# Kernel optimization log

Measured on AMD Instinct MI355X. Metric: run time of the kernel, lower is better.

## Reference

```python
import jax, jax.numpy as jnp
import numpy as np

B, C, H, W = 32, 256, 56, 56
O, K = 512, 3


def setup_inputs() -> dict:
    key = jax.random.key(0)
    kx, kw = jax.random.split(key)
    x = jax.random.normal(kx, (B, C, H, W), dtype=jnp.float32)
    # Ternary weight stored as two disjoint boolean masks of shape (C*K*K, O),
    # matching the torch buffer layout: weight.view(O, C*K*K).t().
    u = jax.random.uniform(kw, (C * K * K, O))
    pos_weight = u < 0.45
    neg_weight = u > 0.55
    return {"x": x, "pos_weight": pos_weight, "neg_weight": neg_weight}


def reference(x, pos_weight, neg_weight):
    # pos/neg masks: (C*K*K, O) bool, disjoint. The torch module computes
    # sum(unfold(x) where pos) - sum(unfold(x) where neg) over the C*K*K axis
    # per output channel, i.e. a conv with ternary weight in {-1, 0, +1}.
    b, c, h, w = x.shape
    ckk, o = pos_weight.shape
    k = int(round((ckk // c) ** 0.5))  # kernel size (square)
    wt = pos_weight.astype(x.dtype) - neg_weight.astype(x.dtype)  # (C*K*K, O)
    # torch unfold orders the patch axis as (C, kh, kw); weight came from
    # view(O, C*K*K).t(), so transposing back gives OIHW layout directly.
    wt = wt.T.reshape(o, c, k, k)
    pad = (k - 1) // 2  # 'same' padding (output reshaped to (b, O, h, w))
    out = jax.lax.conv_general_dilated(
        x, wt,
        window_strides=(1, 1),
        padding=[(pad, pad), (pad, pad)],
        dimension_numbers=("NCHW", "OIHW", "NCHW"),
    )
    return out  # (b, O, h, w)
```

## Files before the change

kernel.cpp:

```cpp
#include <hip/hip_runtime.h>
#include <hip/hip_bf16.h>

#define BB 32
#define CC 256
#define HH 56
#define WW 56
#define OO 512
#define CKK 2304

#define XR 58
#define XC 58
#define XPIX (XR * XC)

#define NY 4
#define NX 28
#define NTILE 112
#define TPC 30
#define TPIX 180
#define BUFB 16384

typedef __bf16 bf16x8 __attribute__((ext_vector_type(8)));
typedef float  f32x4  __attribute__((ext_vector_type(4)));

#define WT_OFF 4096
#define XP_OFF (WT_OFF + (size_t)OO * CKK * 2)

__global__ void detect_bool_width(const unsigned int* __restrict__ pos,
                                  unsigned int* __restrict__ flag) {
    unsigned int v = 0;
    for (int i = threadIdx.x; i < 16384; i += 256) v |= pos[i];
    __shared__ unsigned int red;
    if (threadIdx.x == 0) red = 0u;
    __syncthreads();
    if (v > 1u) atomicOr(&red, 1u);
    __syncthreads();
    if (threadIdx.x == 0) *flag = red;
}

__global__ __launch_bounds__(256) void decode_w(
    const void* __restrict__ posv, const void* __restrict__ negv,
    const unsigned int* __restrict__ flag,
    unsigned short* __restrict__ wt) {
    __shared__ unsigned short lds[64][65];
    int blk = blockIdx.x;
    int ot  = blk & 7;
    int khw = (blk >> 3) % 9;
    int ct  = blk / 72;
    int o0 = ot * 64, c0 = ct * 64;
    int t = threadIdx.x;
    int o_l = t & 63, row4 = t >> 6;
    bool bytes = (*flag != 0u);
#pragma unroll
    for (int r = 0; r < 16; ++r) {
        int c_l = row4 + r * 4;
        long k = (long)(c0 + c_l) * 9 + khw;
        long idx = k * OO + o0 + o_l;
        int p, q;
        if (bytes) { p = ((const unsigned char*)posv)[idx];
                     q = ((const unsigned char*)negv)[idx]; }
        else       { p = ((const int*)posv)[idx];
                     q = ((const int*)negv)[idx]; }
        lds[c_l][o_l] = p ? 0x3F80u : (q ? 0xBF80u : 0u);
    }
    __syncthreads();
#pragma unroll
    for (int r = 0; r < 16; ++r) {
        int o_r = row4 + r * 4;
        int c = c0 + (t & 63);
        wt[(size_t)(o0 + o_r) * CKK + (c >> 5) * 288 + khw * 32 + (c & 31)] =
            lds[t & 63][o_r];
    }
}

__global__ __launch_bounds__(256) void pad_x(const float* __restrict__ x,
                                             unsigned short* __restrict__ xp) {
    int blk = blockIdx.x;
    int b = blk / XR, y = blk - b * XR;
    int t = threadIdx.x;
    unsigned short* rowp = xp + ((size_t)b * XPIX + (size_t)y * XC) * CC;
    if (y == 0 || y == XR - 1) {
        uint4 z = {0, 0, 0, 0};
        for (int i = t; i < XC * CC / 8; i += 256) ((uint4*)rowp)[i] = z;
        return;
    }
    __shared__ float lds[WW][65];
    for (int cb = 0; cb < 4; ++cb) {
        if (cb) __syncthreads();
#pragma unroll
        for (int i = 0; i < 14; ++i) {
            int idx = i * 256 + t;
            int cl = idx / WW, xx = idx - cl * WW;
            lds[xx][cl] =
                x[(((size_t)b * CC + cb * 64 + cl) * HH + (y - 1)) * WW + xx];
        }
        __syncthreads();
#pragma unroll
        for (int i = 0; i < 15; ++i) {
            int idx = i * 256 + t;
            if (idx < XC * 64) {
                int xx = idx >> 6, cl = idx & 63;
                float v = (xx == 0 || xx == XC - 1) ? 0.f : lds[xx - 1][cl];
                __hip_bfloat16 h = __float2bfloat16(v);
                rowp[(size_t)xx * CC + cb * 64 + cl] = *(unsigned short*)&h;
            }
        }
    }
}

__global__ __launch_bounds__(256, 2) void conv_mfma(
    const unsigned short* __restrict__ xp,
    const unsigned short* __restrict__ wt,
    float* __restrict__ out) {
    __shared__ __align__(1024) unsigned short Bs[2 * BUFB / 2];

    int t = threadIdx.x;
    int w = t >> 6, lane = t & 63, lm = lane & 15, lq = lane >> 4;

    int bx = blockIdx.x;
    int mb = (bx >> 3) & 1;
    int gn = ((bx >> 4) << 3) | (bx & 7);
    int b = gn / 28;
    int rem = gn - b * 28;
    int y0 = (rem >> 1) << 2;
    int x0 = (rem & 1) * NX;

    int bofs[7];
#pragma unroll
    for (int nt = 0; nt < 7; ++nt) {
        int n = nt * 16 + lm;
        int ny = n / NX, nx = n - (n / NX) * NX;
        bofs[nt] = (ny * TPC + nx) * 64 + lq * 16;
    }

    const unsigned short* gsrc[3];
    int useg[3];
#pragma unroll
    for (int i = 0; i < 3; ++i) {
        int u = (w * 3 + i) * 64 + lane;
        useg[i] = u;
        int pix = u >> 2, quad = u & 3;
        int py = pix / TPC, px = pix - py * TPC;
        gsrc[i] = xp + ((size_t)b * XPIX + (y0 + py) * XC + (x0 + px)) * CC +
                  quad * 8;
    }
    int ldsseg = (w * 3) * 1024;

    const unsigned short* aptr[4];
#pragma unroll
    for (int mt = 0; mt < 4; ++mt)
        aptr[mt] = wt + (size_t)(mb * 256 + w * 64 + mt * 16 + lm) * CKK + lq * 8;

    f32x4 acc[4][7];
#pragma unroll
    for (int i = 0; i < 4; ++i)
#pragma unroll
        for (int j = 0; j < 7; ++j) acc[i][j] = (f32x4){0.f, 0.f, 0.f, 0.f};

    bf16x8 af[12];

#define STAGE(CHOFF, POFS)                                                     \
    {                                                                          \
        _Pragma("unroll") for (int i = 0; i < 3; ++i) {                        \
            if (useg[i] < TPIX * 4)                                            \
                __builtin_amdgcn_global_load_lds(                              \
                    (const __attribute__((address_space(1))) void*)(gsrc[i] +  \
                                                                    (CHOFF)),  \
                    (__attribute__((address_space(3))) void*)((char*)Bs +      \
                                                              (POFS) + ldsseg +\
                                                              i * 1024),       \
                    16, 0, 0);                                                 \
        }                                                                      \
    }

#define LOADA(CHEL, G)                                                         \
    {                                                                          \
        _Pragma("unroll") for (int j = 0; j < 3; ++j)                          \
            _Pragma("unroll") for (int mt = 0; mt < 4; ++mt)                   \
                af[j * 4 + mt] = *(const bf16x8*)(aptr[mt] + (CHEL) +          \
                                                  ((G) * 3 + j) * 32);         \
    }

#define GRP(G, POFS)                                                           \
    {                                                                          \
        _Pragma("unroll") for (int j = 0; j < 3; ++j) {                        \
            const int khw = (G) * 3 + j;                                       \
            const int kh = khw / 3, kw = khw - kh * 3;                         \
            _Pragma("unroll") for (int nt = 0; nt < 7; ++nt) {                 \
                bf16x8 bfr = *(const bf16x8*)((char*)Bs + (POFS) +             \
                                              (kh * TPC + kw) * 64 + bofs[nt]);\
                _Pragma("unroll") for (int mt = 0; mt < 4; ++mt)               \
                    acc[mt][nt] = __builtin_amdgcn_mfma_f32_16x16x32_bf16(     \
                        af[j * 4 + mt], bfr, acc[mt][nt], 0, 0, 0);            \
            }                                                                  \
        }                                                                      \
    }

    STAGE(0, 0);
    LOADA(0, 0);
    for (int it = 0; it < 4; ++it) {
        __syncthreads();
        STAGE(32, BUFB);
        GRP(0, 0);
        LOADA(0, 1);  GRP(1, 0);
        LOADA(0, 2);  GRP(2, 0);
        LOADA(288, 0);
        __syncthreads();
        if (it < 3) STAGE(64, 0);
        GRP(0, BUFB);
        LOADA(288, 1); GRP(1, BUFB);
        LOADA(288, 2); GRP(2, BUFB);
        if (it < 3) {
#pragma unroll
            for (int mt = 0; mt < 4; ++mt) aptr[mt] += 576;
#pragma unroll
            for (int i = 0; i < 3; ++i) gsrc[i] += 64;
            LOADA(0, 0);
        }
    }
#undef STAGE
#undef LOADA
#undef GRP

#pragma unroll
    for (int mt = 0; mt < 4; ++mt) {
        int o = mb * 256 + w * 64 + mt * 16 + lq * 4;
#pragma unroll
        for (int nt = 0; nt < 7; ++nt) {
            int n = nt * 16 + lm;
            int ny = n / NX, nx = n - (n / NX) * NX;
            size_t base =
                (((size_t)b * OO + o) * HH + (y0 + ny)) * WW + (x0 + nx);
#pragma unroll
            for (int r = 0; r < 4; ++r)
                out[base + (size_t)r * HH * WW] = acc[mt][nt][r];
        }
    }
}

extern "C" void kernel_launch(void* const* d_in, const int* in_sizes, int n_in,
                              void* d_out, int out_size, void* d_ws, size_t ws_size,
                              hipStream_t stream) {
    const float* x   = (const float*)d_in[0];
    const void*  pos = d_in[1];
    const void*  neg = d_in[2];
    float* out = (float*)d_out;

    unsigned int* flag = (unsigned int*)d_ws;
    unsigned short* wt = (unsigned short*)((char*)d_ws + WT_OFF);
    unsigned short* xpad = (unsigned short*)((char*)d_ws + XP_OFF);

    detect_bool_width<<<1, 256, 0, stream>>>((const unsigned int*)pos, flag);
    decode_w<<<288, 256, 0, stream>>>(pos, neg, flag, wt);
    pad_x<<<BB * XR, 256, 0, stream>>>(x, xpad);
    conv_mfma<<<dim3(1792), 256, 0, stream>>>(xpad, wt, out);
}
```

Before: 616.5 us.

## Pad LDS pixel stride and stage input via registers instead of direct LDS loads

Moves staging of the input tile from global_load_lds direct-to-LDS copies to ordinary global loads into registers, followed by explicit ds_write stores spread across the MFMA groups. The LDS pixel stride is padded from 64 to 80 bytes so that B-fragment reads from LDS hit fewer bank conflicts, which the fixed-layout direct loads could not provide. The cost is extra VGPRs to hold the staged data and extra LDS write instructions, which may hurt occupancy or scheduling.

Result: slower. 716.8 us (+16.3%).

```diff
diff --git a/kernel.cpp b/kernel.cpp
--- a/kernel.cpp
+++ b/kernel.cpp
@@ -17,6 +17,7 @@
 #define NTILE 112
 #define TPC 30
 #define TPIX 180
+#define PSTR 80
 #define BUFB 16384
 
 typedef __bf16 bf16x8 __attribute__((ext_vector_type(8)));
@@ -129,21 +130,20 @@
     for (int nt = 0; nt < 7; ++nt) {
         int n = nt * 16 + lm;
         int ny = n / NX, nx = n - (n / NX) * NX;
-        bofs[nt] = (ny * TPC + nx) * 64 + lq * 16;
-    }
-
+        bofs[nt] = (ny * TPC + nx) * PSTR + lq * 16;
+    }
+
+    int u0 = w * 192 + lane;
     const unsigned short* gsrc[3];
-    int useg[3];
 #pragma unroll
     for (int i = 0; i < 3; ++i) {
-        int u = (w * 3 + i) * 64 + lane;
-        useg[i] = u;
-        int pix = u >> 2, quad = u & 3;
+        int u = u0 + 64 * i;
+        int pix = u >> 2, q = u & 3;
         int py = pix / TPC, px = pix - py * TPC;
         gsrc[i] = xp + ((size_t)b * XPIX + (y0 + py) * XC + (x0 + px)) * CC +
-                  quad * 8;
-    }
-    int ldsseg = (w * 3) * 1024;
+                  q * 8;
+    }
+    int wadr0 = (u0 >> 2) * PSTR + (u0 & 3) * 16;
 
     const unsigned short* aptr[4];
 #pragma unroll
@@ -157,19 +157,25 @@
         for (int j = 0; j < 7; ++j) acc[i][j] = (f32x4){0.f, 0.f, 0.f, 0.f};
 
     bf16x8 af[12];
-
-#define STAGE(CHOFF, POFS)                                                     \
-    {                                                                          \
-        _Pragma("unroll") for (int i = 0; i < 3; ++i) {                        \
-            if (useg[i] < TPIX * 4)                                            \
-                __builtin_amdgcn_global_load_lds(                              \
-                    (const __attribute__((address_space(1))) void*)(gsrc[i] +  \
-                                                                    (CHOFF)),  \
-                    (__attribute__((address_space(3))) void*)((char*)Bs +      \
-                                                              (POFS) + ldsseg +\
-                                                              i * 1024),       \
-                    16, 0, 0);                                                 \
-        }                                                                      \
+    bf16x8 s0, s1, s2;
+
+#define GLOAD01(CHOFF)                                                         \
+    {                                                                          \
+        s0 = *(const bf16x8*)(gsrc[0] + (CHOFF));                              \
+        if (u0 < 656) s1 = *(const bf16x8*)(gsrc[1] + (CHOFF));                \
+    }
+#define GLOAD2(CHOFF)                                                          \
+    {                                                                          \
+        if (u0 < 592) s2 = *(const bf16x8*)(gsrc[2] + (CHOFF));                \
+    }
+#define DSW01(POFS)                                                            \
+    {                                                                          \
+        *(bf16x8*)((char*)Bs + (POFS) + wadr0) = s0;                           \
+        if (u0 < 656) *(bf16x8*)((char*)Bs + (POFS) + wadr0 + 1280) = s1;      \
+    }
+#define DSW2(POFS)                                                             \
+    {                                                                          \
+        if (u0 < 592) *(bf16x8*)((char*)Bs + (POFS) + wadr0 + 2560) = s2;      \
     }
 
 #define LOADA(CHEL, G)                                                         \
@@ -187,7 +193,8 @@
             const int kh = khw / 3, kw = khw - kh * 3;                         \
             _Pragma("unroll") for (int nt = 0; nt < 7; ++nt) {                 \
                 bf16x8 bfr = *(const bf16x8*)((char*)Bs + (POFS) +             \
-                                              (kh * TPC + kw) * 64 + bofs[nt]);\
+                                              (kh * TPC + kw) * PSTR +         \
+                                              bofs[nt]);                       \
                 _Pragma("unroll") for (int mt = 0; mt < 4; ++mt)               \
                     acc[mt][nt] = __builtin_amdgcn_mfma_f32_16x16x32_bf16(     \
                         af[j * 4 + mt], bfr, acc[mt][nt], 0, 0, 0);            \
@@ -195,21 +202,29 @@
         }                                                                      \
     }
 
-    STAGE(0, 0);
+    GLOAD01(0); GLOAD2(0);
+    DSW01(0);   DSW2(0);
     LOADA(0, 0);
     for (int it = 0; it < 4; ++it) {
         __syncthreads();
-        STAGE(32, BUFB);
+        GLOAD01(32);
         GRP(0, 0);
-        LOADA(0, 1);  GRP(1, 0);
-        LOADA(0, 2);  GRP(2, 0);
+        LOADA(0, 1); GLOAD2(32);
+        GRP(1, 0);
+        DSW01(BUFB);
+        LOADA(0, 2); GRP(2, 0);
+        DSW2(BUFB);
         LOADA(288, 0);
         __syncthreads();
-        if (it < 3) STAGE(64, 0);
+        if (it < 3) GLOAD01(64);
         GRP(0, BUFB);
-        LOADA(288, 1); GRP(1, BUFB);
+        LOADA(288, 1);
+        if (it < 3) GLOAD2(64);
+        GRP(1, BUFB);
+        if (it < 3) DSW01(0);
         LOADA(288, 2); GRP(2, BUFB);
         if (it < 3) {
+            DSW2(0);
 #pragma unroll
             for (int mt = 0; mt < 4; ++mt) aptr[mt] += 576;
 #pragma unroll
@@ -217,7 +232,10 @@
             LOADA(0, 0);
         }
     }
-#undef STAGE
+#undef GLOAD01
+#undef GLOAD2
+#undef DSW01
+#undef DSW2
 #undef LOADA
 #undef GRP
 
```
